# Performance work log

Measured on AMD Instinct MI355X. Metric: run time of the kernel, lower is better.

Reference implementation:

```python
import jax, jax.numpy as jnp
import numpy as np
import math

SI, VI = 128, 32
H_DIM = 32          # max(vi, vo) for q/k/v GVPs; max(vi, 0)=32 for weight_proj
HEADS = 4
N_ANCHORS = 32
S_H, V_H = SI // HEADS, VI // HEADS  # 32, 8


def _norm_no_nan(x, axis=-1, keepdims=False, eps=1e-8):
    return jnp.sqrt(jnp.maximum(jnp.sum(x * x, axis=axis, keepdims=keepdims), eps))


def _gvp_full(s, v, wh, ws_w, ws_b, wv, wsv_w, wsv_b):
    # GVP with activations=(silu, sigmoid), vector_gate=True, vo>0
    vt = jnp.swapaxes(v, -1, -2)                 # [..., 3, vi]
    vh = vt @ wh.T                               # [..., 3, h]
    vn = _norm_no_nan(vh, axis=-2)               # [..., h]
    s_out = jnp.concatenate([s, vn], -1) @ ws_w.T + ws_b   # [..., so]
    v_out = jnp.swapaxes(vh @ wv.T, -1, -2)      # [..., vo, 3]
    gate = jax.nn.sigmoid(s_out) @ wsv_w.T + wsv_b
    v_out = v_out * jax.nn.sigmoid(gate)[..., None]
    return jax.nn.silu(s_out), v_out


def _gvp_scalar(s, v, wh, ws_w, ws_b):
    # weight_proj: activations=(None, None), vo=0 -> scalar output only
    vt = jnp.swapaxes(v, -1, -2)
    vh = vt @ wh.T
    vn = _norm_no_nan(vh, axis=-2)
    return jnp.concatenate([s, vn], -1) @ ws_w.T + ws_b


def setup_inputs() -> dict:
    key = jax.random.key(0)
    ks = jax.random.split(key, 32)
    N, C = 8192, 16
    inp = {
        's': jax.random.normal(ks[0], (N, C, SI), jnp.float32),
        'v': jax.random.normal(ks[1], (N, C, VI, 3), jnp.float32),
    }

    def lin(k, out_d, in_d):
        return jax.random.normal(k, (out_d, in_d), jnp.float32) / math.sqrt(in_d)

    # weight_proj: GVP((128,32) -> (32,0)), h_dim = max(32,0) = 32
    inp['wp_wh'] = lin(ks[2], H_DIM, VI)
    inp['wp_ws_w'] = lin(ks[3], N_ANCHORS, H_DIM + SI)
    inp['wp_ws_b'] = jnp.zeros((N_ANCHORS,), jnp.float32)
    # to_q / to_k / to_v: GVP((128,32) -> (128,32)), h_dim = 32
    i = 4
    for p in ('q', 'k', 'vp'):
        inp[f'{p}_wh'] = lin(ks[i], H_DIM, VI); i += 1
        inp[f'{p}_ws_w'] = lin(ks[i], SI, H_DIM + SI); i += 1
        inp[f'{p}_ws_b'] = jnp.zeros((SI,), jnp.float32)
        inp[f'{p}_wv'] = lin(ks[i], VI, H_DIM); i += 1
        inp[f'{p}_wsv_w'] = lin(ks[i], VI, SI); i += 1
        inp[f'{p}_wsv_b'] = jnp.zeros((VI,), jnp.float32)
    return inp


def reference(s, v, wp_wh, wp_ws_w, wp_ws_b,
              q_wh, q_ws_w, q_ws_b, q_wv, q_wsv_w, q_wsv_b,
              k_wh, k_ws_w, k_ws_b, k_wv, k_wsv_w, k_wsv_b,
              vp_wh, vp_ws_w, vp_ws_b, vp_wv, vp_wsv_w, vp_wsv_b):
    N, C = s.shape[:2]
    H, r = HEADS, N_ANCHORS

    # Compress: softmax over nodes -> r anchors
    p_logits = _gvp_scalar(s, v, wp_wh, wp_ws_w, wp_ws_b)       # [N, C, r]
    p_weights = jax.nn.softmax(p_logits, axis=0)
    s_global = jnp.einsum('nca,ncs->acs', p_weights, s)          # [r, C, si]
    v_global = jnp.einsum('nca,ncvd->acvd', p_weights, v)        # [r, C, vi, 3]

    s_q, v_q = _gvp_full(s, v, q_wh, q_ws_w, q_ws_b, q_wv, q_wsv_w, q_wsv_b)
    s_k, v_k = _gvp_full(s_global, v_global, k_wh, k_ws_w, k_ws_b, k_wv, k_wsv_w, k_wsv_b)
    s_val, v_val = _gvp_full(s_global, v_global, vp_wh, vp_ws_w, vp_ws_b, vp_wv, vp_wsv_w, vp_wsv_b)

    # split heads
    qs = s_q.reshape(N, C, H, S_H); qv = v_q.reshape(N, C, H, V_H, 3)
    ks_ = s_k.reshape(r, C, H, S_H); kv = v_k.reshape(r, C, H, V_H, 3)
    vs = s_val.reshape(r, C, H, S_H); vv = v_val.reshape(r, C, H, V_H, 3)

    s_dot = jnp.einsum('nchs,rchs->nrch', qs, ks_)
    v_dot = jnp.einsum('nchvd,rchvd->nrch', qv, kv)
    energy = (s_dot + v_dot) / math.sqrt(S_H + V_H)
    alpha = jax.nn.softmax(energy, axis=1)                       # softmax over anchors r
    # dropout is identity at inference

    out_s = jnp.einsum('nrch,rchs->nchs', alpha, vs).reshape(N, C, SI)
    out_v = jnp.einsum('nrch,rchvd->nchvd', alpha, vv).reshape(N, C, VI, 3)
    return out_s, out_v
```

## Files before the change

kernel.cpp:

```cpp
#include <hip/hip_runtime.h>
#include <stdint.h>

typedef unsigned short ushort_t;
typedef __attribute__((ext_vector_type(8))) short short8;
typedef __attribute__((ext_vector_type(4))) float float4v;

static constexpr int N_=8192, C_=16;

static constexpr long OFF_LOGITS = 0;
static constexpr long OFF_PM  = 4194304;
static constexpr long OFF_PS  = 4210688;
static constexpr long OFF_M   = 4227072;
static constexpr long OFF_INV = 4227584;
static constexpr long OFF_SGL = 4228096;
static constexpr long OFF_VGL = 4293632;
static constexpr long OFF_KATT= 4342784;
static constexpr long OFF_VATT= 4408320;
static constexpr long OFF_WF  = 4473856;
static constexpr long WF_WHQ=0, WF_WHWP=1024, WF_KWH=2048, WF_KWS=3072, WF_KWV=23552,
  WF_KWSV=24576, WF_VWH=28672, WF_VWS=29696, WF_VWV=50176, WF_VWSV=51200,
  WF_B1=55296 , WF_BG=70656 ,
  WF_BV=72704 ;

static constexpr long VH_B   = 67108864;
static constexpr long AVN_B  = 92274688;

__device__ __forceinline__ uint32_t f2bf(float f){
  uint32_t u = __float_as_uint(f);
  return (u + 0x7FFFu + ((u>>16)&1u)) >> 16;
}

__device__ __forceinline__ void split_bf(float f, short& hi, short& lo){
  uint32_t u = __float_as_uint(f);
  uint32_t h = (u + 0x7FFFu + ((u>>16)&1u)) >> 16;
  hi = (short)h;
  float fh = __uint_as_float(h << 16);
  float r = f - fh;
  uint32_t u2 = __float_as_uint(r);
  lo = (short)((u2 + 0x7FFFu + ((u2>>16)&1u)) >> 16);
}

__device__ __forceinline__ long katt_idx(int c, int h, int k, int r){
  int kt=k>>5, kk=k&31, nt=r>>4;
  int lane=((kk>>3)<<4)|(r&15), j=kk&7;
  return ((((long)(c*4+h)*2+kt)*2+nt)*64+lane)*8+j;
}
__device__ __forceinline__ long vatt_idx(int c, int h, int r, int n2){
  int nt=n2>>4;
  int lane=((r>>3)<<4)|(n2&15), j=r&7;
  return (((long)(c*4+h)*4+nt)*64+lane)*8+j;
}

__global__ void k0_prep(const float* __restrict__ wpwh, const float* __restrict__ wpws,
    const float* __restrict__ qwh, const float* __restrict__ qws, const float* __restrict__ qwv,
    const float* __restrict__ qwsv, const float* __restrict__ kwh, const float* __restrict__ kws,
    const float* __restrict__ kwv, const float* __restrict__ kwsv, const float* __restrict__ vwh,
    const float* __restrict__ vws, const float* __restrict__ vwv, const float* __restrict__ vwsv,
    float* __restrict__ wsf){
  int job=blockIdx.x, t=threadIdx.x;
  float* W = wsf + OFF_WF;
  auto tr=[&](const float* src, float* dst, int O, int J){
    for(int idx=t; idx<O*J; idx+=blockDim.x){int o=idx/J, j=idx-o*J; dst[j*O+o]=src[idx];}
  };
  switch(job){
    case 0: tr(qwh,  W+WF_WHQ, 32,32); break;
    case 1: tr(wpwh, W+WF_WHWP,32,32); break;
    case 2: tr(kwh,  W+WF_KWH, 32,32); break;
    case 3: tr(kws,  W+WF_KWS, 128,160); break;
    case 4: tr(kwv,  W+WF_KWV, 32,32); break;
    case 5: tr(kwsv, W+WF_KWSV,32,128); break;
    case 6: tr(vwh,  W+WF_VWH, 32,32); break;
    case 7: tr(vws,  W+WF_VWS, 128,160); break;
    case 8: tr(vwv,  W+WF_VWV, 32,32); break;
    case 9: tr(vwsv, W+WF_VWSV,32,128); break;
    case 10: {
      ushort_t* dst=(ushort_t*)(W+WF_B1);
      for(int idx=t; idx<30720; idx+=blockDim.x){
        int j=idx&7, lane=(idx>>3)&63, tn=idx>>9, nt=tn%10, kt=tn/10;
        int k=kt*32+((lane>>4)<<3)+j, n=nt*16+(lane&15);
        float val;
        if(k<128)       val = (n<128)? qws[n*160+k]            : wpws[(n-128)*160+k];
        else if(k<160)  val = (n<128)? qws[n*160+k]            : 0.f;
        else            val = (n<128)? 0.f                     : wpws[(n-128)*160+(k-32)];
        dst[idx]=(ushort_t)f2bf(val);
      } } break;
    case 11: {
      ushort_t* dst=(ushort_t*)(W+WF_BG);
      for(int idx=t; idx<4096; idx+=blockDim.x){
        int j=idx&7, lane=(idx>>3)&63, tn=idx>>9, nt=tn&1, kt=tn>>1;
        int k=kt*32+((lane>>4)<<3)+j, n=nt*16+(lane&15);
        dst[idx]=(ushort_t)f2bf(qwsv[n*128+k]);
      } } break;
    case 12: {
      ushort_t* dst=(ushort_t*)(W+WF_BV);
      for(int idx=t; idx<1024; idx+=blockDim.x){
        int j=idx&7, lane=(idx>>3)&63, nt=idx>>9;
        int k=((lane>>4)<<3)+j, n=nt*16+(lane&15);
        dst[idx]=(ushort_t)f2bf(qwv[n*32+k]);
      } } break;
  }
}

__global__ __launch_bounds__(256) void kA_vn(const float* __restrict__ v,
    const float* __restrict__ wsf, ushort_t* __restrict__ vh_s, ushort_t* __restrict__ avn_s){
  __shared__ float whq[1024], whwp[1024];
  __shared__ float vb[4][96];
  int t=threadIdx.x, wave=t>>6, lane=t&63;
  for(int i=t;i<1024;i+=256){ whq[i]=wsf[OFF_WF+WF_WHQ+i]; whwp[i]=wsf[OFF_WF+WF_WHWP+i]; }
  __syncthreads();
  int h=lane&31, half=lane>>5;
  for(int it=0; it<32; it++){
    long inst = ((long)blockIdx.x*4 + wave)*32 + it;
    if(lane<48) ((float2*)vb[wave])[lane] = ((const float2*)v)[inst*48+lane];
    float d0=0,d1=0,d2=0;
    for(int i=half*16;i<half*16+16;i++){ float w=whq[i*32+h];
      d0+=vb[wave][3*i]*w; d1+=vb[wave][3*i+1]*w; d2+=vb[wave][3*i+2]*w; }
    d0+=__shfl_xor(d0,32,64); d1+=__shfl_xor(d1,32,64); d2+=__shfl_xor(d2,32,64);
    if(lane<32){
      float vn=sqrtf(fmaxf(d0*d0+d1*d1+d2*d2,1e-8f));
      avn_s[inst*64+h]=(ushort_t)f2bf(vn);
      vh_s[(inst*3+0)*32+h]=(ushort_t)f2bf(d0);
      vh_s[(inst*3+1)*32+h]=(ushort_t)f2bf(d1);
      vh_s[(inst*3+2)*32+h]=(ushort_t)f2bf(d2);
    }
    float e0=0,e1=0,e2=0;
    for(int i=half*16;i<half*16+16;i++){ float w=whwp[i*32+h];
      e0+=vb[wave][3*i]*w; e1+=vb[wave][3*i+1]*w; e2+=vb[wave][3*i+2]*w; }
    e0+=__shfl_xor(e0,32,64); e1+=__shfl_xor(e1,32,64); e2+=__shfl_xor(e2,32,64);
    if(lane<32){
      float vn=sqrtf(fmaxf(e0*e0+e1*e1+e2*e2,1e-8f));
      avn_s[inst*64+32+h]=(ushort_t)f2bf(vn);
    }
  }
}

__global__ __launch_bounds__(256) void kB_gemm(const float* __restrict__ s,
    float* __restrict__ wsf,
    const float* __restrict__ qwsb, const float* __restrict__ wpwsb,
    const float* __restrict__ qwsvb,
    ushort_t* __restrict__ qatt, const ushort_t* __restrict__ vh_s,
    const ushort_t* __restrict__ avn_s){
  __shared__ ushort_t sigl[4][16*136];
  __shared__ float    gsigl[4][16*33];
  int t=threadIdx.x, wave=t>>6, lane=t&63;
  int l15=lane&15, lq=lane>>4;
  long m0 = ((long)blockIdx.x*4 + wave)*16;
  const short8* B1 = (const short8*)(wsf + OFF_WF + WF_B1);
  const short8* BG = (const short8*)(wsf + OFF_WF + WF_BG);
  const short8* BV = (const short8*)(wsf + OFF_WF + WF_BV);
  float4v acc[10];
  #pragma unroll
  for(int i=0;i<10;i++) acc[i]=(float4v){0.f,0.f,0.f,0.f};
  #pragma unroll
  for(int kt=0;kt<4;kt++){
    const float* sp = s + (m0+l15)*128 + kt*32 + lq*8;
    float4 f0=*(const float4*)sp, f1=*(const float4*)(sp+4);
    short8 a;
    a[0]=(short)f2bf(f0.x); a[1]=(short)f2bf(f0.y); a[2]=(short)f2bf(f0.z); a[3]=(short)f2bf(f0.w);
    a[4]=(short)f2bf(f1.x); a[5]=(short)f2bf(f1.y); a[6]=(short)f2bf(f1.z); a[7]=(short)f2bf(f1.w);
    #pragma unroll
    for(int nt=0;nt<10;nt++)
      acc[nt]=__builtin_amdgcn_mfma_f32_16x16x32_bf16(a, B1[(kt*10+nt)*64+lane], acc[nt],0,0,0);
  }
  #pragma unroll
  for(int kt=4;kt<6;kt++){
    short8 a = *(const short8*)&avn_s[(m0+l15)*64 + (kt-4)*32 + lq*8];
    #pragma unroll
    for(int nt=0;nt<10;nt++)
      acc[nt]=__builtin_amdgcn_mfma_f32_16x16x32_bf16(a, B1[(kt*10+nt)*64+lane], acc[nt],0,0,0);
  }
  ushort_t* sl = sigl[wave]; float* gl = gsigl[wave];
  #pragma unroll
  for(int nt=0;nt<8;nt++){
    float b = qwsb[nt*16+l15];
    #pragma unroll
    for(int reg=0;reg<4;reg++){
      float x = acc[nt][reg] + b;
      float sg = 1.f/(1.f+__expf(-x));
      int row = lq*4+reg, col=nt*16+l15;
      long inst = m0+row;
      qatt[(inst*4 + (col>>5))*64 + (col&31)] = (ushort_t)f2bf(x*sg);
      sl[row*136+col] = (ushort_t)f2bf(sg);
    }
  }
  #pragma unroll
  for(int nt=8;nt<10;nt++){
    float b = wpwsb[(nt-8)*16+l15];
    #pragma unroll
    for(int reg=0;reg<4;reg++){
      long inst=m0+lq*4+reg;
      wsf[OFF_LOGITS + inst*32 + (nt-8)*16+l15] = acc[nt][reg]+b;
    }
  }
  __syncthreads();
  float4v g0=(float4v){0.f,0.f,0.f,0.f}, g1=g0;
  #pragma unroll
  for(int kt=0;kt<4;kt++){
    short8 a = *(const short8*)&sl[l15*136 + kt*32 + lq*8];
    g0=__builtin_amdgcn_mfma_f32_16x16x32_bf16(a, BG[(kt*2+0)*64+lane], g0,0,0,0);
    g1=__builtin_amdgcn_mfma_f32_16x16x32_bf16(a, BG[(kt*2+1)*64+lane], g1,0,0,0);
  }
  {
    float b0 = qwsvb[l15], b1 = qwsvb[16+l15];
    #pragma unroll
    for(int reg=0;reg<4;reg++){
      int row=lq*4+reg;
      gl[row*33 + l15]    = 1.f/(1.f+__expf(-(g0[reg]+b0)));
      gl[row*33 + 16+l15] = 1.f/(1.f+__expf(-(g1[reg]+b1)));
    }
  }
  __syncthreads();
  #pragma unroll
  for(int tt=0;tt<3;tt++){
    short8 a = *(const short8*)&vh_s[(m0*3 + tt*16 + l15)*32 + lq*8];
    float4v v0=(float4v){0.f,0.f,0.f,0.f}, v1=v0;
    v0=__builtin_amdgcn_mfma_f32_16x16x32_bf16(a, BV[0*64+lane], v0,0,0,0);
    v1=__builtin_amdgcn_mfma_f32_16x16x32_bf16(a, BV[1*64+lane], v1,0,0,0);
    #pragma unroll
    for(int nt2=0;nt2<2;nt2++){
      #pragma unroll
      for(int reg=0;reg<4;reg++){
        int lr = tt*16 + lq*4 + reg;
        int il = lr/3, d = lr - il*3;
        int o = nt2*16+l15;
        float val = (nt2? v1[reg] : v0[reg]) * gl[il*33+o];
        long inst = m0 + il;
        qatt[(inst*4 + (o>>3))*64 + 32 + (o&7)*3 + d] = (ushort_t)f2bf(val);
      }
    }
  }
}

__global__ __launch_bounds__(256) void k2a_stats(float* __restrict__ ws){
  int c = blockIdx.x; int chunk = blockIdx.y;
  int t=threadIdx.x; int i=t>>5, a=t&31;
  const float* L = ws + OFF_LOGITS;
  float m=-1e30f, sum=0.f;
  for(int k2=0;k2<32;k2++){
    int n = chunk*256 + k2*8 + i;
    float x = L[((long)n*16 + c)*32 + a];
    float mn = fmaxf(m,x);
    sum = sum*__expf(m-mn) + __expf(x-mn);
    m = mn;
  }
  __shared__ float sm[8][32], ss[8][32];
  sm[i][a]=m; ss[i][a]=sum;
  __syncthreads();
  if(t<32){
    float M=sm[0][t], S=ss[0][t];
    for(int q=1;q<8;q++){
      float mq=sm[q][t], sq_=ss[q][t];
      float mn=fmaxf(M,mq); S=S*__expf(M-mn)+sq_*__expf(mq-mn); M=mn;
    }
    ws[OFF_PM + (chunk*16+c)*32 + t]=M;
    ws[OFF_PS + (chunk*16+c)*32 + t]=S;
  }
}

__global__ __launch_bounds__(256) void k2b_merge(float* __restrict__ ws){
  int t = blockIdx.x*256 + threadIdx.x;
  if(t>=512) return;
  int c=t>>5, a=t&31;
  float M=-1e30f, S=0.f;
  for(int ch=0; ch<32; ch++){
    float mq=ws[OFF_PM+(ch*16+c)*32+a], sq_=ws[OFF_PS+(ch*16+c)*32+a];
    float mn=fmaxf(M,mq); S=S*__expf(M-mn)+sq_*__expf(mq-mn); M=mn;
  }
  ws[OFF_M + t]=M; ws[OFF_INV + t]=1.0f/S;
}

template<int NMT, bool ISV>
__device__ __forceinline__ void k3_body(const float* __restrict__ X, int d0,
    const float* __restrict__ L, float M0, float M1, float I0, float I1,
    int c, int nb0, int l15, int lq, float* __restrict__ ws){
  constexpr int XP = ISV ? 96 : 128;
  float4v acc[NMT][2];
  #pragma unroll
  for(int mi=0;mi<NMT;mi++){
    acc[mi][0]=(float4v){0.f,0.f,0.f,0.f};
    acc[mi][1]=(float4v){0.f,0.f,0.f,0.f};
  }
  #pragma unroll
  for(int kt=0;kt<4;kt++){
    int nb = nb0 + kt*32 + lq*8;
    short8 bh0, bl0, bh1, bl1;
    #pragma unroll
    for(int j=0;j<8;j++){
      long ro = ((long)(nb+j)*16 + c)*32;
      float w0 = __expf(L[ro + l15]      - M0) * I0;
      float w1 = __expf(L[ro + 16 + l15] - M1) * I1;
      short h_, lo_;
      split_bf(w0, h_, lo_); bh0[j]=h_; bl0[j]=lo_;
      split_bf(w1, h_, lo_); bh1[j]=h_; bl1[j]=lo_;
    }
    #pragma unroll
    for(int mi=0;mi<NMT;mi++){
      short8 ah, al_;
      #pragma unroll
      for(int j=0;j<8;j++){
        float f = X[((long)(nb+j)*16 + c)*XP + d0 + mi*16 + l15];
        short h_, lo_;
        split_bf(f, h_, lo_); ah[j]=h_; al_[j]=lo_;
      }
      acc[mi][0]=__builtin_amdgcn_mfma_f32_16x16x32_bf16(ah,  bh0, acc[mi][0],0,0,0);
      acc[mi][0]=__builtin_amdgcn_mfma_f32_16x16x32_bf16(al_, bh0, acc[mi][0],0,0,0);
      acc[mi][0]=__builtin_amdgcn_mfma_f32_16x16x32_bf16(ah,  bl0, acc[mi][0],0,0,0);
      acc[mi][1]=__builtin_amdgcn_mfma_f32_16x16x32_bf16(ah,  bh1, acc[mi][1],0,0,0);
      acc[mi][1]=__builtin_amdgcn_mfma_f32_16x16x32_bf16(al_, bh1, acc[mi][1],0,0,0);
      acc[mi][1]=__builtin_amdgcn_mfma_f32_16x16x32_bf16(ah,  bl1, acc[mi][1],0,0,0);
    }
  }
  #pragma unroll
  for(int mi=0;mi<NMT;mi++){
    #pragma unroll
    for(int nt=0;nt<2;nt++){
      int a = nt*16 + l15;
      #pragma unroll
      for(int reg=0;reg<4;reg++){
        int dloc = d0 + mi*16 + lq*4 + reg;
        if(ISV) atomicAdd(&ws[OFF_VGL + ((long)a*16+c)*96  + dloc], acc[mi][nt][reg]);
        else    atomicAdd(&ws[OFF_SGL + ((long)a*16+c)*128 + dloc], acc[mi][nt][reg]);
      }
    }
  }
}

__global__ __launch_bounds__(256) void k3_globals(const float* __restrict__ s,
    const float* __restrict__ v, float* __restrict__ ws){
  int c = blockIdx.x & 15; int chunk = blockIdx.x >> 4;
  int t=threadIdx.x, wave=t>>6, lane=t&63;
  int l15=lane&15, lq=lane>>4;
  const float* L = ws + OFF_LOGITS;
  float M0 = ws[OFF_M   + c*32 + l15],      M1 = ws[OFF_M   + c*32 + 16 + l15];
  float I0 = ws[OFF_INV + c*32 + l15],      I1 = ws[OFF_INV + c*32 + 16 + l15];
  int nb0 = chunk*128;
  if(wave==0)      k3_body<4,false>(s, 0,   L, M0,M1,I0,I1, c, nb0, l15, lq, ws);
  else if(wave==1) k3_body<4,false>(s, 64,  L, M0,M1,I0,I1, c, nb0, l15, lq, ws);
  else if(wave==2) k3_body<3,true >(v, 0,   L, M0,M1,I0,I1, c, nb0, l15, lq, ws);
  else             k3_body<3,true >(v, 48,  L, M0,M1,I0,I1, c, nb0, l15, lq, ws);
}

__global__ __launch_bounds__(64) void k4_kvgvp(float* __restrict__ wsf,
    const float* __restrict__ k_wsb, const float* __restrict__ k_wsvb,
    const float* __restrict__ v_wsb, const float* __restrict__ v_wsvb){
  int a = blockIdx.x >> 4, c = blockIdx.x & 15;
  int lane = threadIdx.x;
  __shared__ __align__(16) float cat[160];
  __shared__ __align__(16) float vb2[96];
  __shared__ float vhb[96];
  __shared__ __align__(16) float sg[128];
  const float* W = wsf + OFF_WF;
  ushort_t* katt = (ushort_t*)(wsf + OFF_KATT);
  ushort_t* vatt = (ushort_t*)(wsf + OFF_VATT);
  long inst = (long)a*16 + c;
  ((float2*)cat)[lane] = ((const float2*)(wsf+OFF_SGL))[inst*64 + lane];
  if(lane<48) ((float2*)vb2)[lane] = ((const float2*)(wsf+OFF_VGL))[inst*48 + lane];
  __syncthreads();
  if(a==0){
    for(int idx=lane; idx<1024; idx+=64){
      int h2=idx&3, kk=56+((idx>>2)&7), r=idx>>5;
      katt[katt_idx(c,h2,kk,r)]=0;
      vatt[vatt_idx(c,h2,r,kk)]=0;
    }
  }
  int h = lane&31, half = lane>>5;
  for(int p=0;p<2;p++){
    const float* wht  = W + (p? WF_VWH  : WF_KWH);
    const float* wst  = W + (p? WF_VWS  : WF_KWS);
    const float* wvt  = W + (p? WF_VWV  : WF_KWV);
    const float* wsvt = W + (p? WF_VWSV : WF_KWSV);
    const float* bs   = p? v_wsb : k_wsb;
    const float* bsv  = p? v_wsvb : k_wsvb;
    float d0=0.f,d1=0.f,d2=0.f;
    for(int i=half*16; i<half*16+16; i++){
      float w_=wht[i*32+h];
      d0+=vb2[3*i]*w_; d1+=vb2[3*i+1]*w_; d2+=vb2[3*i+2]*w_;
    }
    d0 += __shfl_xor(d0,32,64); d1 += __shfl_xor(d1,32,64); d2 += __shfl_xor(d2,32,64);
    if(lane<32){
      cat[128+h] = sqrtf(fmaxf(d0*d0+d1*d1+d2*d2, 1e-8f));
      vhb[3*h]=d0; vhb[3*h+1]=d1; vhb[3*h+2]=d2;
    }
    __syncthreads();
    float a0=bs[lane], a1=bs[lane+64];
    for(int j=0;j<160;j+=4){
      float4 c4=*((float4*)&cat[j]);
      a0 += c4.x*wst[j*128+lane]      + c4.y*wst[(j+1)*128+lane]
          + c4.z*wst[(j+2)*128+lane]  + c4.w*wst[(j+3)*128+lane];
      a1 += c4.x*wst[j*128+64+lane]   + c4.y*wst[(j+1)*128+64+lane]
          + c4.z*wst[(j+2)*128+64+lane]+ c4.w*wst[(j+3)*128+64+lane];
    }
    float sig0=1.f/(1.f+__expf(-a0)), sig1=1.f/(1.f+__expf(-a1));
    float silu0=a0*sig0, silu1=a1*sig1;
    sg[lane]=sig0; sg[lane+64]=sig1;
    {
      int o=lane, hh2=o>>5, k=o&31;
      if(p==0) katt[katt_idx(c,hh2,k,a)] = (ushort_t)f2bf(silu0);
      else     vatt[vatt_idx(c,hh2,a,k)] = (ushort_t)f2bf(silu0);
    }
    {
      int o=lane+64, hh2=o>>5, k=o&31;
      if(p==0) katt[katt_idx(c,hh2,k,a)] = (ushort_t)f2bf(silu1);
      else     vatt[vatt_idx(c,hh2,a,k)] = (ushort_t)f2bf(silu1);
    }
    __syncthreads();
    float gacc=0.f;
    for(int o=half*64; o<half*64+64; o+=4){
      float4 s4_=*((float4*)&sg[o]);
      gacc += s4_.x*wsvt[o*32+h]+s4_.y*wsvt[(o+1)*32+h]+s4_.z*wsvt[(o+2)*32+h]+s4_.w*wsvt[(o+3)*32+h];
    }
    gacc += __shfl_xor(gacc,32,64);
    float sgate = 1.f/(1.f+__expf(-(gacc + bsv[h])));
    float e0=0.f,e1=0.f,e2=0.f;
    for(int hh=half*16; hh<half*16+16; hh++){
      float w_=wvt[hh*32+h];
      e0+=vhb[3*hh]*w_; e1+=vhb[3*hh+1]*w_; e2+=vhb[3*hh+2]*w_;
    }
    e0+=__shfl_xor(e0,32,64); e1+=__shfl_xor(e1,32,64); e2+=__shfl_xor(e2,32,64);
    if(lane<32){
      int hh2=lane>>3, oo=lane&7;
      float vals[3]={e0*sgate, e1*sgate, e2*sgate};
      #pragma unroll
      for(int d=0;d<3;d++){
        if(p==0) katt[katt_idx(c,hh2,32+oo*3+d,a)] = (ushort_t)f2bf(vals[d]);
        else     vatt[vatt_idx(c,hh2,a,32+oo*3+d)] = (ushort_t)f2bf(vals[d]);
      }
    }
    __syncthreads();
  }
}

__global__ __launch_bounds__(256) void k5_attn(const float* __restrict__ wsf, float* out){
  __shared__ ushort_t al[4][4*16*40];
  int t=threadIdx.x, wave=t>>6, lane=t&63;
  int l15=lane&15, lq=lane>>4;
  int c=blockIdx.y;
  long n0 = ((long)blockIdx.x*4+wave)*16;
  const ushort_t* qatt = (const ushort_t*)out;
  const short8* KA = (const short8*)(wsf + OFF_KATT);
  const short8* VA = (const short8*)(wsf + OFF_VATT);
  const float scale = 0.15811388300841897f;
  float4v e[4][2];
  #pragma unroll
  for(int h=0;h<4;h++){ e[h][0]=(float4v){0.f,0.f,0.f,0.f}; e[h][1]=e[h][0]; }
  #pragma unroll
  for(int h=0;h<4;h++){
    #pragma unroll
    for(int kt=0;kt<2;kt++){
      short8 a = *(const short8*)&qatt[(((n0+l15)*16 + c)*4 + h)*64 + kt*32 + lq*8];
      e[h][0]=__builtin_amdgcn_mfma_f32_16x16x32_bf16(a, KA[(((c*4+h)*2+kt)*2+0)*64+lane], e[h][0],0,0,0);
      e[h][1]=__builtin_amdgcn_mfma_f32_16x16x32_bf16(a, KA[(((c*4+h)*2+kt)*2+1)*64+lane], e[h][1],0,0,0);
    }
  }
  ushort_t* alw = al[wave];
  #pragma unroll
  for(int h=0;h<4;h++){
    #pragma unroll
    for(int reg=0;reg<4;reg++){
      float a0=e[h][0][reg]*scale, a1=e[h][1][reg]*scale;
      float m=fmaxf(a0,a1);
      m=fmaxf(m,__shfl_xor(m,1,64)); m=fmaxf(m,__shfl_xor(m,2,64));
      m=fmaxf(m,__shfl_xor(m,4,64)); m=fmaxf(m,__shfl_xor(m,8,64));
      float p0=__expf(a0-m), p1=__expf(a1-m);
      float sum=p0+p1;
      sum+=__shfl_xor(sum,1,64); sum+=__shfl_xor(sum,2,64);
      sum+=__shfl_xor(sum,4,64); sum+=__shfl_xor(sum,8,64);
      float inv=1.f/sum;
      int row=lq*4+reg;
      alw[h*640 + row*40 + l15]      = (ushort_t)f2bf(p0*inv);
      alw[h*640 + row*40 + 16 + l15] = (ushort_t)f2bf(p1*inv);
    }
  }
  __syncthreads();
  float* outv = out + 16777216;
  #pragma unroll
  for(int h=0;h<4;h++){
    short8 a = *(const short8*)&alw[h*640 + l15*40 + lq*8];
    #pragma unroll
    for(int nt=0;nt<4;nt++){
      float4v o_=(float4v){0.f,0.f,0.f,0.f};
      o_=__builtin_amdgcn_mfma_f32_16x16x32_bf16(a, VA[((c*4+h)*4+nt)*64+lane], o_,0,0,0);
      #pragma unroll
      for(int reg=0;reg<4;reg++){
        int n2=nt*16+l15, row=lq*4+reg;
        long inst=(n0+row)*16+c;
        float val=o_[reg];
        if(n2<32)      out[inst*128 + h*32+n2]=val;
        else if(n2<56) outv[inst*96 + h*24 + n2-32]=val;
      }
    }
  }
}

extern "C" void kernel_launch(void* const* d_in, const int* in_sizes, int n_in,
                              void* d_out, int out_size, void* d_ws, size_t ws_size,
                              hipStream_t stream){
  (void)in_sizes; (void)n_in; (void)out_size; (void)ws_size;
  const float* s = (const float*)d_in[0];
  const float* v = (const float*)d_in[1];
  float* wsf = (float*)d_ws;
  float* out = (float*)d_out;
  ushort_t* qatt  = (ushort_t*)d_out;
  ushort_t* vh_s  = (ushort_t*)((char*)d_out + VH_B);
  ushort_t* avn_s = (ushort_t*)((char*)d_out + AVN_B);
  (void)hipMemsetAsync((char*)d_ws + OFF_SGL*sizeof(float), 0, (size_t)(65536+49152)*sizeof(float), stream);
  k0_prep<<<13,256,0,stream>>>(
      (const float*)d_in[2],(const float*)d_in[3],
      (const float*)d_in[5],(const float*)d_in[6],(const float*)d_in[8],(const float*)d_in[9],
      (const float*)d_in[11],(const float*)d_in[12],(const float*)d_in[14],(const float*)d_in[15],
      (const float*)d_in[17],(const float*)d_in[18],(const float*)d_in[20],(const float*)d_in[21], wsf);
  kA_vn<<<1024,256,0,stream>>>(v, wsf, vh_s, avn_s);
  kB_gemm<<<2048,256,0,stream>>>(s, wsf, (const float*)d_in[7], (const float*)d_in[4],
                                 (const float*)d_in[10], qatt, vh_s, avn_s);
  k2a_stats<<<dim3(16,32),256,0,stream>>>(wsf);
  k2b_merge<<<2,256,0,stream>>>(wsf);
  k3_globals<<<1024,256,0,stream>>>(s, v, wsf);
  k4_kvgvp<<<512,64,0,stream>>>(wsf, (const float*)d_in[13], (const float*)d_in[16],
                                (const float*)d_in[19], (const float*)d_in[22]);
  k5_attn<<<dim3(128,16),256,0,stream>>>(wsf, out);
}
```

Before: 583.8 us.

## Replace atomic accumulation of anchor globals with partial buffers and a reduction kernel

The globals kernel no longer accumulates its MFMA results with scalar float atomics into shared s_global/v_global rows. Each chunk instead writes its partial sums as float4 stores into a per-chunk scratch area placed in the output buffer. A new reduction kernel then sums the 64 chunk partials into the workspace, which also removes the need for the zeroing memset. The cost is an extra launch and roughly 29 MB of partial-buffer traffic. The scratch region reuses output memory that earlier kernels also use, which is only safe if that data is no longer read at this point.

Result: faster. 499.1 us (-14.5%).

```diff
diff --git a/kernel.cpp b/kernel.cpp
--- a/kernel.cpp
+++ b/kernel.cpp
@@ -24,6 +24,9 @@
 
 static constexpr long VH_B   = 67108864;
 static constexpr long AVN_B  = 92274688;
+static constexpr long PART_B = 67108864;
+static constexpr long PART_ROWSZ = 224;
+static constexpr long PART_CHUNKSZ = 512*224;
 
 __device__ __forceinline__ uint32_t f2bf(float f){
   uint32_t u = __float_as_uint(f);
@@ -270,9 +273,9 @@
 }
 
 template<int NMT, bool ISV>
-__device__ __forceinline__ void k3_body(const float* __restrict__ X, int d0,
+__device__ __forceinline__ void k3_body(const float* __restrict__ X, int dx0, int pb0,
     const float* __restrict__ L, float M0, float M1, float I0, float I1,
-    int c, int nb0, int l15, int lq, float* __restrict__ ws){
+    int c, int nb0, int l15, int lq, float* __restrict__ partc){
   constexpr int XP = ISV ? 96 : 128;
   float4v acc[NMT][2];
   #pragma unroll
@@ -298,7 +301,7 @@
       short8 ah, al_;
       #pragma unroll
       for(int j=0;j<8;j++){
-        float f = X[((long)(nb+j)*16 + c)*XP + d0 + mi*16 + l15];
+        float f = X[((long)(nb+j)*16 + c)*XP + dx0 + mi*16 + l15];
         short h_, lo_;
         split_bf(f, h_, lo_); ah[j]=h_; al_[j]=lo_;
       }
@@ -315,18 +318,15 @@
     #pragma unroll
     for(int nt=0;nt<2;nt++){
       int a = nt*16 + l15;
-      #pragma unroll
-      for(int reg=0;reg<4;reg++){
-        int dloc = d0 + mi*16 + lq*4 + reg;
-        if(ISV) atomicAdd(&ws[OFF_VGL + ((long)a*16+c)*96  + dloc], acc[mi][nt][reg]);
-        else    atomicAdd(&ws[OFF_SGL + ((long)a*16+c)*128 + dloc], acc[mi][nt][reg]);
-      }
+      long row = (long)(a*16 + c);
+      float4 val = make_float4(acc[mi][nt][0], acc[mi][nt][1], acc[mi][nt][2], acc[mi][nt][3]);
+      *(float4*)&partc[row*PART_ROWSZ + pb0 + mi*16 + lq*4] = val;
     }
   }
 }
 
 __global__ __launch_bounds__(256) void k3_globals(const float* __restrict__ s,
-    const float* __restrict__ v, float* __restrict__ ws){
+    const float* __restrict__ v, const float* __restrict__ ws, float* __restrict__ part){
   int c = blockIdx.x & 15; int chunk = blockIdx.x >> 4;
   int t=threadIdx.x, wave=t>>6, lane=t&63;
   int l15=lane&15, lq=lane>>4;
@@ -334,10 +334,22 @@
   float M0 = ws[OFF_M   + c*32 + l15],      M1 = ws[OFF_M   + c*32 + 16 + l15];
   float I0 = ws[OFF_INV + c*32 + l15],      I1 = ws[OFF_INV + c*32 + 16 + l15];
   int nb0 = chunk*128;
-  if(wave==0)      k3_body<4,false>(s, 0,   L, M0,M1,I0,I1, c, nb0, l15, lq, ws);
-  else if(wave==1) k3_body<4,false>(s, 64,  L, M0,M1,I0,I1, c, nb0, l15, lq, ws);
-  else if(wave==2) k3_body<3,true >(v, 0,   L, M0,M1,I0,I1, c, nb0, l15, lq, ws);
-  else             k3_body<3,true >(v, 48,  L, M0,M1,I0,I1, c, nb0, l15, lq, ws);
+  float* partc = part + (long)chunk*PART_CHUNKSZ;
+  if(wave==0)      k3_body<4,false>(s, 0,  0,   L, M0,M1,I0,I1, c, nb0, l15, lq, partc);
+  else if(wave==1) k3_body<4,false>(s, 64, 64,  L, M0,M1,I0,I1, c, nb0, l15, lq, partc);
+  else if(wave==2) k3_body<3,true >(v, 0,  128, L, M0,M1,I0,I1, c, nb0, l15, lq, partc);
+  else             k3_body<3,true >(v, 48, 176, L, M0,M1,I0,I1, c, nb0, l15, lq, partc);
+}
+
+__global__ __launch_bounds__(256) void k3r_reduce(const float* __restrict__ part,
+    float* __restrict__ ws){
+  int idx = blockIdx.x*256 + threadIdx.x;
+  int ac = idx / 224, d = idx - ac*224;
+  float sum = 0.f;
+  #pragma unroll 8
+  for(int ch=0; ch<64; ch++) sum += part[(long)ch*PART_CHUNKSZ + idx];
+  if(d<128) ws[OFF_SGL + (long)ac*128 + d]       = sum;
+  else      ws[OFF_VGL + (long)ac*96  + (d-128)] = sum;
 }
 
 __global__ __launch_bounds__(64) void k4_kvgvp(float* __restrict__ wsf,
@@ -503,7 +515,7 @@
   ushort_t* qatt  = (ushort_t*)d_out;
   ushort_t* vh_s  = (ushort_t*)((char*)d_out + VH_B);
   ushort_t* avn_s = (ushort_t*)((char*)d_out + AVN_B);
-  (void)hipMemsetAsync((char*)d_ws + OFF_SGL*sizeof(float), 0, (size_t)(65536+49152)*sizeof(float), stream);
+  float* part = (float*)((char*)d_out + PART_B);
   k0_prep<<<13,256,0,stream>>>(
       (const float*)d_in[2],(const float*)d_in[3],
       (const float*)d_in[5],(const float*)d_in[6],(const float*)d_in[8],(const float*)d_in[9],
@@ -514,7 +526,8 @@
                                  (const float*)d_in[10], qatt, vh_s, avn_s);
   k2a_stats<<<dim3(16,32),256,0,stream>>>(wsf);
   k2b_merge<<<2,256,0,stream>>>(wsf);
-  k3_globals<<<1024,256,0,stream>>>(s, v, wsf);
+  k3_globals<<<1024,256,0,stream>>>(s, v, wsf, part);
+  k3r_reduce<<<448,256,0,stream>>>(part, wsf);
   k4_kvgvp<<<512,64,0,stream>>>(wsf, (const float*)d_in[13], (const float*)d_in[16],
                                 (const float*)d_in[19], (const float*)d_in[22]);
   k5_attn<<<dim3(128,16),256,0,stream>>>(wsf, out);
```
